# Optimization experiments

Measured on AMD Instinct MI355X. Metric: run time of the kernel, lower is better.

Reference implementation:

```python
import jax, jax.numpy as jnp
import numpy as np

N_QUBITS = 8


def setup_inputs() -> dict:
    key = jax.random.key(0)
    k1, k2, k3, k4 = jax.random.split(key, 4)
    B, S, E, F = 4, 4096, 1024, 4096
    x = jax.random.normal(k1, (B, S, E), dtype=jnp.float32)
    theta = jax.random.normal(k2, (N_QUBITS,), dtype=jnp.float32)
    # nn.Linear default init scale ~ 1/sqrt(fan_in)
    w1 = jax.random.normal(k3, (F, N_QUBITS), dtype=jnp.float32) / np.sqrt(N_QUBITS)
    w2 = jax.random.normal(k4, (E, F), dtype=jnp.float32) / np.sqrt(F)
    return {"x": x, "theta": theta, "w1": w1, "w2": w2}


def reference(x, theta, w1, w2):
    # Quantum circuit per wire i: |0> -RX(x_i)-> -RY(theta_i)-> <Z>
    # No entangling gates, so <Z_i> = cos(x_i) * cos(theta_i) exactly.
    q_vecs = jnp.cos(x[..., :N_QUBITS]) * jnp.cos(theta)  # [B,S,nq]
    h = jax.nn.relu(jnp.einsum('bsq,fq->bsf', q_vecs, w1))  # [B,S,F]
    # dropout is identity in eval mode
    out = jnp.einsum('bsf,ef->bse', h, w2)  # [B,S,E]
    return out
```

## Files before the change

### kernel.cpp

```cpp
#include <hip/hip_runtime.h>
#include <hip/hip_bf16.h>


#define M_TOTAL 16384
#define E_DIM 1024
#define F_DIM 4096
#define NQ 8

typedef __attribute__((ext_vector_type(8))) short bf16x8;
typedef __attribute__((ext_vector_type(8))) unsigned short ushort8;
typedef __attribute__((ext_vector_type(4))) float f32x4;

__device__ __forceinline__ unsigned short f2bf(float f) {
  union { float f; unsigned u; } c; c.f = f;
  unsigned u = c.u + (0x7fffu + ((c.u >> 16) & 1u));
  return (unsigned short)(u >> 16);
}

__global__ __launch_bounds__(256) void w2cvt_kernel(
    const float* __restrict__ w2, unsigned short* __restrict__ w2bf) {
  size_t i = ((size_t)blockIdx.x * 256 + threadIdx.x) * 8;
  float v[8];
  *(float4*)&v[0] = *(const float4*)&w2[i];
  *(float4*)&v[4] = *(const float4*)&w2[i + 4];
  ushort8 p;
#pragma unroll
  for (int j = 0; j < 8; ++j) p[j] = f2bf(v[j]);
  *(ushort8*)&w2bf[i] = p;
}

__global__ __launch_bounds__(256) void qrelu_kernel(
    const float* __restrict__ x, const float* __restrict__ theta,
    const float* __restrict__ w1, unsigned short* __restrict__ A, int m_base) {
  __shared__ float qv[32][NQ];
  const int t = threadIdx.x;
  const int m0 = m_base + blockIdx.x * 32;
  {
    const int ml = t >> 3, q = t & 7;
    float xv = x[(size_t)(m0 + ml) * 1024 + q];
    qv[ml][q] = cosf(xv) * cosf(theta[q]);
  }
  __syncthreads();

  for (int oi = 0; oi < 2; ++oi) {
    const int o = t + oi * 256;
    float w[64];
#pragma unroll
    for (int i = 0; i < 16; ++i)
      *(float4*)&w[i * 4] = *(const float4*)&w1[o * 64 + i * 4];
    for (int ml = 0; ml < 32; ++ml) {
      ushort8 pk;
#pragma unroll
      for (int j = 0; j < 8; ++j) {
        float s = 0.f;
#pragma unroll
        for (int q = 0; q < NQ; ++q) s = fmaf(qv[ml][q], w[j * 8 + q], s);
        pk[j] = f2bf(s > 0.f ? s : 0.f);
      }
      *(ushort8*)&A[(size_t)(m0 - m_base + ml) * F_DIM + o * 8] = pk;
    }
  }
}

#define PHASE(ms, ns, B, W) do { \
  __builtin_amdgcn_s_barrier(); \
  asm volatile("s_waitcnt lgkmcnt(" #W ")" ::: "memory"); \
  __builtin_amdgcn_sched_barrier(0); \
  __builtin_amdgcn_s_setprio(1); \
  _Pragma("unroll") \
  for (int mt2 = 0; mt2 < 4; ++mt2) { \
    _Pragma("unroll") \
    for (int nt2 = 0; nt2 < 2; ++nt2) { \
      _Pragma("unroll") \
      for (int kk = 0; kk < 2; ++kk) { \
        acc[(ms) * 4 + mt2][(ns) * 2 + nt2] = \
            __builtin_amdgcn_mfma_f32_16x16x32_bf16( \
                af[mt2][kk], B[nt2][kk], acc[(ms) * 4 + mt2][(ns) * 2 + nt2], \
                0, 0, 0); \
      } } } \
  __builtin_amdgcn_s_setprio(0); \
  __builtin_amdgcn_s_barrier(); \
} while (0)

#define RD_A(buf, ms) do { \
  _Pragma("unroll") \
  for (int mt2 = 0; mt2 < 4; ++mt2) { \
    af[mt2][0] = *(const bf16x8*)&asW[(buf) * 16384 + (ms) * 4096 + mt2 * 1024 + aO0]; \
    af[mt2][1] = *(const bf16x8*)&asW[(buf) * 16384 + (ms) * 4096 + mt2 * 1024 + aO1]; \
  } } while (0)

#define RD_B(buf, ns, B) do { \
  _Pragma("unroll") \
  for (int nt2 = 0; nt2 < 2; ++nt2) { \
    B[nt2][0] = *(const bf16x8*)&bsW[(buf) * 16384 + (ns) * 2048 + nt2 * 1024 + bO0]; \
    B[nt2][1] = *(const bf16x8*)&bsW[(buf) * 16384 + (ns) * 2048 + nt2 * 1024 + bO1]; \
  } } while (0)

__global__ __launch_bounds__(512, 2) void gemm8_kernel(
    const unsigned short* __restrict__ Abf, const unsigned short* __restrict__ w2bf,
    float* __restrict__ out, int m_base) {
  __shared__ __align__(16) unsigned short As[2][2][128 * 64];
  __shared__ __align__(16) unsigned short Bs[2][2][128 * 64];

  const int tid = threadIdx.x;
  const int lane = tid & 63;
  const int wid = tid >> 6;
  const int wr = wid >> 2;
  const int wc = wid & 3;

  const int nwg = gridDim.x;
  const int bid = blockIdx.x;
  const int qq = nwg >> 3, rr = nwg & 7;
  const int xcd = bid & 7, sub = bid >> 3;
  const int wgid =
      (xcd < rr ? xcd * (qq + 1) : rr * (qq + 1) + (xcd - rr) * qq) + sub;
  const int mb = wgid >> 2;
  const int nb = wgid & 3;

  const unsigned short* Ag = Abf + (size_t)mb * 256 * F_DIM;
  const unsigned short* Bg = w2bf + (size_t)nb * 256 * F_DIM;

  f32x4 acc[8][4] = {};
  bf16x8 af[4][2], blo[2][2], bhi[2][2];

  const int hi4 = lane >> 4, l7 = lane & 7, l15 = lane & 15;
  const int aO0 = l15 * 64 + ((hi4 ^ l7) << 3);
  const int aO1 = aO0 ^ 32;
  const int bO0 = ((wc & 1) * 64 + l15) * 64 + ((hi4 ^ l7) << 3);
  const int bO1 = bO0 ^ 32;
  const unsigned short* asW = &As[0][wr][0];
  const unsigned short* bsW = &Bs[0][wc >> 1][0];

  const int srow = tid >> 3;
  const int sc = (tid & 7) ^ (srow & 7);
  const unsigned short* pA0 = Ag + (size_t)(srow)*F_DIM + sc * 8;
  const unsigned short* pA1 = Ag + (size_t)(64 + srow) * F_DIM + sc * 8;
  const unsigned short* pA2 = Ag + (size_t)(128 + srow) * F_DIM + sc * 8;
  const unsigned short* pA3 = Ag + (size_t)(192 + srow) * F_DIM + sc * 8;
  const unsigned short* pB0 = Bg + (size_t)(srow)*F_DIM + sc * 8;
  const unsigned short* pB1 = Bg + (size_t)(64 + srow) * F_DIM + sc * 8;
  const unsigned short* pB2 = Bg + (size_t)(128 + srow) * F_DIM + sc * 8;
  const unsigned short* pB3 = Bg + (size_t)(192 + srow) * F_DIM + sc * 8;

  auto stA = [&](int buf, int half, const unsigned short*& r0,
                 const unsigned short*& r1) {
    unsigned short* d = &As[buf][half][wid * 512];
    __builtin_amdgcn_global_load_lds(
        (const __attribute__((address_space(1))) void*)r0,
        (__attribute__((address_space(3))) void*)d, 16, 0, 0);
    __builtin_amdgcn_global_load_lds(
        (const __attribute__((address_space(1))) void*)r1,
        (__attribute__((address_space(3))) void*)(d + 4096), 16, 0, 0);
    r0 += 64; r1 += 64;
  };
  auto stB = [&](int buf, int half, const unsigned short*& r0,
                 const unsigned short*& r1) {
    unsigned short* d = &Bs[buf][half][wid * 512];
    __builtin_amdgcn_global_load_lds(
        (const __attribute__((address_space(1))) void*)r0,
        (__attribute__((address_space(3))) void*)d, 16, 0, 0);
    __builtin_amdgcn_global_load_lds(
        (const __attribute__((address_space(1))) void*)r1,
        (__attribute__((address_space(3))) void*)(d + 4096), 16, 0, 0);
    r0 += 64; r1 += 64;
  };

  stB(0, 0, pB0, pB1); stB(0, 1, pB2, pB3);
  stA(0, 0, pA0, pA1); stA(0, 1, pA2, pA3);
  stB(1, 0, pB0, pB1); stB(1, 1, pB2, pB3);
  stA(1, 0, pA0, pA1);
  asm volatile("s_waitcnt vmcnt(6)" ::: "memory");
  __builtin_amdgcn_s_barrier();

#pragma unroll 1
  for (int it = 0; it < F_DIM / 128; ++it) {
    const bool notlast = (it != F_DIM / 128 - 1);
    RD_A(0, 0); RD_B(0, 0, blo); RD_B(0, 1, bhi);
    stA(1, 1, pA2, pA3);
    PHASE(0, 0, blo, 4);
    PHASE(0, 1, bhi, 0);
    RD_A(0, 1);
    if (notlast) stB(0, 0, pB0, pB1);
    PHASE(1, 1, bhi, 0);
    if (notlast) {
      stB(0, 1, pB2, pB3);
      stA(0, 0, pA0, pA1);
      asm volatile("s_waitcnt vmcnt(6)" ::: "memory");
    } else {
      asm volatile("s_waitcnt vmcnt(0)" ::: "memory");
    }
    PHASE(1, 0, blo, 0);
    RD_A(1, 0); RD_B(1, 0, blo); RD_B(1, 1, bhi);
    if (notlast) stA(0, 1, pA2, pA3);
    PHASE(0, 0, blo, 4);
    PHASE(0, 1, bhi, 0);
    RD_A(1, 1);
    if (notlast) stB(1, 0, pB0, pB1);
    PHASE(1, 1, bhi, 0);
    if (notlast) {
      stB(1, 1, pB2, pB3);
      stA(1, 0, pA0, pA1);
      asm volatile("s_waitcnt vmcnt(6)" ::: "memory");
    }
    PHASE(1, 0, blo, 0);
  }

  const int cl = lane & 15, rg = lane >> 4;
  float* ob = out + (size_t)(m_base + mb * 256 + wr * 128) * E_DIM + nb * 256 +
              wc * 64 + cl;
#pragma unroll
  for (int mt = 0; mt < 8; ++mt)
#pragma unroll
    for (int r = 0; r < 4; ++r) {
      float* orow = ob + (size_t)(mt * 16 + rg * 4 + r) * E_DIM;
#pragma unroll
      for (int nt = 0; nt < 4; ++nt) orow[nt * 16] = acc[mt][nt][r];
    }
}

extern "C" void kernel_launch(void* const* d_in, const int* in_sizes, int n_in,
                              void* d_out, int out_size, void* d_ws, size_t ws_size,
                              hipStream_t stream) {
  const float* x = (const float*)d_in[0];
  const float* theta = (const float*)d_in[1];
  const float* w1 = (const float*)d_in[2];
  const float* w2 = (const float*)d_in[3];
  float* out = (float*)d_out;

  unsigned short* w2bf = (unsigned short*)d_ws;
  unsigned short* A = w2bf + (size_t)E_DIM * F_DIM;

  size_t abytes = ws_size - (size_t)E_DIM * F_DIM * 2;
  size_t maxrows = abytes / ((size_t)F_DIM * 2);
  int Mc = (int)((maxrows / 256) * 256);
  if (Mc > M_TOTAL) Mc = M_TOTAL;
  if (Mc < 256) Mc = 256;

  w2cvt_kernel<<<E_DIM * F_DIM / 2048, 256, 0, stream>>>(w2, w2bf);

  for (int mb = 0; mb < M_TOTAL; mb += Mc) {
    int rows = M_TOTAL - mb < Mc ? M_TOTAL - mb : Mc;
    qrelu_kernel<<<rows / 32, 256, 0, stream>>>(x, theta, w1, A, mb);
    gemm8_kernel<<<(rows / 256) * 4, 512, 0, stream>>>(A, w2bf, out, mb);
  }
}
```

Measured before the change: 167.3 us.

## Switch GEMM to 32x32x16 MFMA with reworked LDS pipeline schedule

Replaces the 16x16x32 bf16 MFMA tiling with 32x32x16 MFMA tiles, so each wave holds 4x2 accumulators of 16 floats. The LDS fragment read pattern, swizzle offsets and epilogue store mapping change to match. The double-buffered schedule is restructured into K-substeps with ping-pong register fragments and a full vmcnt/lgkmcnt sync before restaging each buffer. The aim is fewer MFMA issues and fewer LDS reads per FLOP. In exchange it adds full-drain sync points that may expose global load latency.

Result: no change. 167.4 us (+0.1%).

```diff
diff --git a/kernel.cpp b/kernel.cpp
--- a/kernel.cpp
+++ b/kernel.cpp
@@ -9,7 +9,7 @@
 
 typedef __attribute__((ext_vector_type(8))) short bf16x8;
 typedef __attribute__((ext_vector_type(8))) unsigned short ushort8;
-typedef __attribute__((ext_vector_type(4))) float f32x4;
+typedef __attribute__((ext_vector_type(16))) float f32x16;
 
 __device__ __forceinline__ unsigned short f2bf(float f) {
   union { float f; unsigned u; } c; c.f = f;
@@ -62,45 +62,62 @@
   }
 }
 
-#define PHASE(ms, ns, B, W) do { \
-  __builtin_amdgcn_s_barrier(); \
-  asm volatile("s_waitcnt lgkmcnt(" #W ")" ::: "memory"); \
-  __builtin_amdgcn_sched_barrier(0); \
+#define READ_STEP(b, aO, bO, pp) do { \
+  fA[pp][0] = *(const bf16x8*)&As[(b)*16384 + 0*2048 + (aO)]; \
+  fA[pp][1] = *(const bf16x8*)&As[(b)*16384 + 1*2048 + (aO)]; \
+  fA[pp][2] = *(const bf16x8*)&As[(b)*16384 + 2*2048 + (aO)]; \
+  fA[pp][3] = *(const bf16x8*)&As[(b)*16384 + 3*2048 + (aO)]; \
+  fB[pp][0] = *(const bf16x8*)&Bs[(b)*16384 + 0*2048 + (bO)]; \
+  fB[pp][1] = *(const bf16x8*)&Bs[(b)*16384 + 1*2048 + (bO)]; \
+} while (0)
+
+#define MFMA_STEP(pp) do { \
   __builtin_amdgcn_s_setprio(1); \
   _Pragma("unroll") \
-  for (int mt2 = 0; mt2 < 4; ++mt2) { \
+  for (int mt = 0; mt < 4; ++mt) \
     _Pragma("unroll") \
-    for (int nt2 = 0; nt2 < 2; ++nt2) { \
-      _Pragma("unroll") \
-      for (int kk = 0; kk < 2; ++kk) { \
-        acc[(ms) * 4 + mt2][(ns) * 2 + nt2] = \
-            __builtin_amdgcn_mfma_f32_16x16x32_bf16( \
-                af[mt2][kk], B[nt2][kk], acc[(ms) * 4 + mt2][(ns) * 2 + nt2], \
-                0, 0, 0); \
-      } } } \
+    for (int nt = 0; nt < 2; ++nt) \
+      acc[mt][nt] = __builtin_amdgcn_mfma_f32_32x32x16_bf16( \
+          fA[pp][mt], fB[pp][nt], acc[mt][nt], 0, 0, 0); \
   __builtin_amdgcn_s_setprio(0); \
+} while (0)
+
+#define W6 do { \
+  asm volatile("s_waitcnt lgkmcnt(6)" ::: "memory"); \
+  __builtin_amdgcn_sched_barrier(0); \
+} while (0)
+
+#define SYNC_POINT do { \
+  asm volatile("s_waitcnt vmcnt(0) lgkmcnt(0)" ::: "memory"); \
   __builtin_amdgcn_s_barrier(); \
 } while (0)
 
-#define RD_A(buf, ms) do { \
-  _Pragma("unroll") \
-  for (int mt2 = 0; mt2 < 4; ++mt2) { \
-    af[mt2][0] = *(const bf16x8*)&asW[(buf) * 16384 + (ms) * 4096 + mt2 * 1024 + aO0]; \
-    af[mt2][1] = *(const bf16x8*)&asW[(buf) * 16384 + (ms) * 4096 + mt2 * 1024 + aO1]; \
-  } } while (0)
-
-#define RD_B(buf, ns, B) do { \
-  _Pragma("unroll") \
-  for (int nt2 = 0; nt2 < 2; ++nt2) { \
-    B[nt2][0] = *(const bf16x8*)&bsW[(buf) * 16384 + (ns) * 2048 + nt2 * 1024 + bO0]; \
-    B[nt2][1] = *(const bf16x8*)&bsW[(buf) * 16384 + (ns) * 2048 + nt2 * 1024 + bO1]; \
-  } } while (0)
-
-__global__ __launch_bounds__(512, 2) void gemm8_kernel(
+#define STAGE(b) do { \
+  __builtin_amdgcn_global_load_lds((const __attribute__((address_space(1))) void*)pA0, \
+      (__attribute__((address_space(3))) void*)&As[(b)*16384 + 0*4096 + wid*512], 16, 0, 0); \
+  __builtin_amdgcn_global_load_lds((const __attribute__((address_space(1))) void*)pA1, \
+      (__attribute__((address_space(3))) void*)&As[(b)*16384 + 1*4096 + wid*512], 16, 0, 0); \
+  __builtin_amdgcn_global_load_lds((const __attribute__((address_space(1))) void*)pA2, \
+      (__attribute__((address_space(3))) void*)&As[(b)*16384 + 2*4096 + wid*512], 16, 0, 0); \
+  __builtin_amdgcn_global_load_lds((const __attribute__((address_space(1))) void*)pA3, \
+      (__attribute__((address_space(3))) void*)&As[(b)*16384 + 3*4096 + wid*512], 16, 0, 0); \
+  __builtin_amdgcn_global_load_lds((const __attribute__((address_space(1))) void*)pB0, \
+      (__attribute__((address_space(3))) void*)&Bs[(b)*16384 + 0*4096 + wid*512], 16, 0, 0); \
+  __builtin_amdgcn_global_load_lds((const __attribute__((address_space(1))) void*)pB1, \
+      (__attribute__((address_space(3))) void*)&Bs[(b)*16384 + 1*4096 + wid*512], 16, 0, 0); \
+  __builtin_amdgcn_global_load_lds((const __attribute__((address_space(1))) void*)pB2, \
+      (__attribute__((address_space(3))) void*)&Bs[(b)*16384 + 2*4096 + wid*512], 16, 0, 0); \
+  __builtin_amdgcn_global_load_lds((const __attribute__((address_space(1))) void*)pB3, \
+      (__attribute__((address_space(3))) void*)&Bs[(b)*16384 + 3*4096 + wid*512], 16, 0, 0); \
+  pA0 += 64; pA1 += 64; pA2 += 64; pA3 += 64; \
+  pB0 += 64; pB1 += 64; pB2 += 64; pB3 += 64; \
+} while (0)
+
+__global__ __launch_bounds__(512, 2) void gemm32_kernel(
     const unsigned short* __restrict__ Abf, const unsigned short* __restrict__ w2bf,
     float* __restrict__ out, int m_base) {
-  __shared__ __align__(16) unsigned short As[2][2][128 * 64];
-  __shared__ __align__(16) unsigned short Bs[2][2][128 * 64];
+  __shared__ __align__(16) unsigned short As[2 * 16384];
+  __shared__ __align__(16) unsigned short Bs[2 * 16384];
 
   const int tid = threadIdx.x;
   const int lane = tid & 63;
@@ -120,16 +137,20 @@
   const unsigned short* Ag = Abf + (size_t)mb * 256 * F_DIM;
   const unsigned short* Bg = w2bf + (size_t)nb * 256 * F_DIM;
 
-  f32x4 acc[8][4] = {};
-  bf16x8 af[4][2], blo[2][2], bhi[2][2];
-
-  const int hi4 = lane >> 4, l7 = lane & 7, l15 = lane & 15;
-  const int aO0 = l15 * 64 + ((hi4 ^ l7) << 3);
-  const int aO1 = aO0 ^ 32;
-  const int bO0 = ((wc & 1) * 64 + l15) * 64 + ((hi4 ^ l7) << 3);
-  const int bO1 = bO0 ^ 32;
-  const unsigned short* asW = &As[0][wr][0];
-  const unsigned short* bsW = &Bs[0][wc >> 1][0];
+  f32x16 acc[4][2] = {};
+  bf16x8 fA[2][4], fB[2][2];
+
+  const int hi = lane >> 5, l31 = lane & 31, l7 = lane & 7;
+  const int aBase = wr * 8192 + l31 * 64;
+  const int aO0 = aBase + (((hi + 0) ^ l7) << 3);
+  const int aO1 = aBase + (((hi + 2) ^ l7) << 3);
+  const int aO2 = aBase + (((hi + 4) ^ l7) << 3);
+  const int aO3 = aBase + (((hi + 6) ^ l7) << 3);
+  const int bBase = (wc >> 1) * 8192 + ((wc & 1) * 64 + l31) * 64;
+  const int bO0 = bBase + (((hi + 0) ^ l7) << 3);
+  const int bO1 = bBase + (((hi + 2) ^ l7) << 3);
+  const int bO2 = bBase + (((hi + 4) ^ l7) << 3);
+  const int bO3 = bBase + (((hi + 6) ^ l7) << 3);
 
   const int srow = tid >> 3;
   const int sc = (tid & 7) ^ (srow & 7);
@@ -142,80 +163,50 @@
   const unsigned short* pB2 = Bg + (size_t)(128 + srow) * F_DIM + sc * 8;
   const unsigned short* pB3 = Bg + (size_t)(192 + srow) * F_DIM + sc * 8;
 
-  auto stA = [&](int buf, int half, const unsigned short*& r0,
-                 const unsigned short*& r1) {
-    unsigned short* d = &As[buf][half][wid * 512];
-    __builtin_amdgcn_global_load_lds(
-        (const __attribute__((address_space(1))) void*)r0,
-        (__attribute__((address_space(3))) void*)d, 16, 0, 0);
-    __builtin_amdgcn_global_load_lds(
-        (const __attribute__((address_space(1))) void*)r1,
-        (__attribute__((address_space(3))) void*)(d + 4096), 16, 0, 0);
-    r0 += 64; r1 += 64;
-  };
-  auto stB = [&](int buf, int half, const unsigned short*& r0,
-                 const unsigned short*& r1) {
-    unsigned short* d = &Bs[buf][half][wid * 512];
-    __builtin_amdgcn_global_load_lds(
-        (const __attribute__((address_space(1))) void*)r0,
-        (__attribute__((address_space(3))) void*)d, 16, 0, 0);
-    __builtin_amdgcn_global_load_lds(
-        (const __attribute__((address_space(1))) void*)r1,
-        (__attribute__((address_space(3))) void*)(d + 4096), 16, 0, 0);
-    r0 += 64; r1 += 64;
-  };
-
-  stB(0, 0, pB0, pB1); stB(0, 1, pB2, pB3);
-  stA(0, 0, pA0, pA1); stA(0, 1, pA2, pA3);
-  stB(1, 0, pB0, pB1); stB(1, 1, pB2, pB3);
-  stA(1, 0, pA0, pA1);
-  asm volatile("s_waitcnt vmcnt(6)" ::: "memory");
+  STAGE(0);
+  STAGE(1);
+  asm volatile("s_waitcnt vmcnt(8)" ::: "memory");
   __builtin_amdgcn_s_barrier();
+  READ_STEP(0, aO0, bO0, 0);
 
 #pragma unroll 1
-  for (int it = 0; it < F_DIM / 128; ++it) {
-    const bool notlast = (it != F_DIM / 128 - 1);
-    RD_A(0, 0); RD_B(0, 0, blo); RD_B(0, 1, bhi);
-    stA(1, 1, pA2, pA3);
-    PHASE(0, 0, blo, 4);
-    PHASE(0, 1, bhi, 0);
-    RD_A(0, 1);
-    if (notlast) stB(0, 0, pB0, pB1);
-    PHASE(1, 1, bhi, 0);
-    if (notlast) {
-      stB(0, 1, pB2, pB3);
-      stA(0, 0, pA0, pA1);
-      asm volatile("s_waitcnt vmcnt(6)" ::: "memory");
-    } else {
-      asm volatile("s_waitcnt vmcnt(0)" ::: "memory");
+  for (int it = 0; it < 32; ++it) {
+    const bool nl = (it < 31);
+    READ_STEP(0, aO1, bO1, 1);
+    W6; MFMA_STEP(0);
+    READ_STEP(0, aO2, bO2, 0);
+    W6; MFMA_STEP(1);
+    READ_STEP(0, aO3, bO3, 1);
+    W6; MFMA_STEP(0);
+    SYNC_POINT;
+    if (nl) STAGE(0);
+    READ_STEP(1, aO0, bO0, 0);
+    W6; MFMA_STEP(1);
+    READ_STEP(1, aO1, bO1, 1);
+    W6; MFMA_STEP(0);
+    READ_STEP(1, aO2, bO2, 0);
+    W6; MFMA_STEP(1);
+    READ_STEP(1, aO3, bO3, 1);
+    W6; MFMA_STEP(0);
+    SYNC_POINT;
+    if (nl) {
+      STAGE(1);
+      READ_STEP(0, aO0, bO0, 0);
     }
-    PHASE(1, 0, blo, 0);
-    RD_A(1, 0); RD_B(1, 0, blo); RD_B(1, 1, bhi);
-    if (notlast) stA(0, 1, pA2, pA3);
-    PHASE(0, 0, blo, 4);
-    PHASE(0, 1, bhi, 0);
-    RD_A(1, 1);
-    if (notlast) stB(1, 0, pB0, pB1);
-    PHASE(1, 1, bhi, 0);
-    if (notlast) {
-      stB(1, 1, pB2, pB3);
-      stA(1, 0, pA0, pA1);
-      asm volatile("s_waitcnt vmcnt(6)" ::: "memory");
-    }
-    PHASE(1, 0, blo, 0);
-  }
-
-  const int cl = lane & 15, rg = lane >> 4;
+    W6; MFMA_STEP(1);
+  }
+
   float* ob = out + (size_t)(m_base + mb * 256 + wr * 128) * E_DIM + nb * 256 +
-              wc * 64 + cl;
-#pragma unroll
-  for (int mt = 0; mt < 8; ++mt)
-#pragma unroll
-    for (int r = 0; r < 4; ++r) {
-      float* orow = ob + (size_t)(mt * 16 + rg * 4 + r) * E_DIM;
-#pragma unroll
-      for (int nt = 0; nt < 4; ++nt) orow[nt * 16] = acc[mt][nt][r];
-    }
+              wc * 64 + l31;
+#pragma unroll
+  for (int mt = 0; mt < 4; ++mt)
+#pragma unroll
+    for (int nt = 0; nt < 2; ++nt)
+#pragma unroll
+      for (int r = 0; r < 16; ++r) {
+        const int row = mt * 32 + (r & 3) + 8 * (r >> 2) + 4 * hi;
+        ob[(size_t)row * E_DIM + nt * 32] = acc[mt][nt][r];
+      }
 }
 
 extern "C" void kernel_launch(void* const* d_in, const int* in_sizes, int n_in,
@@ -241,6 +232,6 @@
   for (int mb = 0; mb < M_TOTAL; mb += Mc) {
     int rows = M_TOTAL - mb < Mc ? M_TOTAL - mb : Mc;
     qrelu_kernel<<<rows / 32, 256, 0, stream>>>(x, theta, w1, A, mb);
-    gemm8_kernel<<<(rows / 256) * 4, 512, 0, stream>>>(A, w2bf, out, mb);
-  }
-}
+    gemm32_kernel<<<(rows / 256) * 4, 512, 0, stream>>>(A, w2bf, out, mb);
+  }
+}
```

## Double-buffer LDS fragment registers and cut barriers in GEMM main loop

Applied to the files above, without the earlier changes.

The main GEMM loop now alternates between two register sets for the A and B-low fragments, so the LDS reads for the next phase are issued before the current phase's MFMAs. It drops the trailing barrier from each phase and reorders the global-to-LDS staging, with adjusted vmcnt/lgkmcnt wait counts. The aim is to hide LDS read latency behind MFMA work and lower synchronisation overhead. In exchange it uses more VGPRs, which may threaten the two-blocks-per-CU occupancy, and relies on hand-tuned wait counts whose correctness is fragile.

Result: slower. 221.8 us (+32.6%).

```diff
diff --git a/kernel.cpp b/kernel.cpp
--- a/kernel.cpp
+++ b/kernel.cpp
@@ -62,8 +62,12 @@
   }
 }
 
-#define PHASE(ms, ns, B, W) do { \
-  __builtin_amdgcn_s_barrier(); \
+#define BAR __builtin_amdgcn_s_barrier()
+#define SB __builtin_amdgcn_sched_barrier(0)
+#define VM(n) asm volatile("s_waitcnt vmcnt(" #n ")" ::: "memory")
+
+#define PHASE(AF, BF, ms, ns, W) do { \
+  BAR; \
   asm volatile("s_waitcnt lgkmcnt(" #W ")" ::: "memory"); \
   __builtin_amdgcn_sched_barrier(0); \
   __builtin_amdgcn_s_setprio(1); \
@@ -75,25 +79,25 @@
       for (int kk = 0; kk < 2; ++kk) { \
         acc[(ms) * 4 + mt2][(ns) * 2 + nt2] = \
             __builtin_amdgcn_mfma_f32_16x16x32_bf16( \
-                af[mt2][kk], B[nt2][kk], acc[(ms) * 4 + mt2][(ns) * 2 + nt2], \
+                AF[mt2][kk], BF[nt2][kk], acc[(ms) * 4 + mt2][(ns) * 2 + nt2], \
                 0, 0, 0); \
       } } } \
   __builtin_amdgcn_s_setprio(0); \
-  __builtin_amdgcn_s_barrier(); \
+  __builtin_amdgcn_sched_barrier(0); \
 } while (0)
 
-#define RD_A(buf, ms) do { \
+#define RD_A(buf, ms, AF) do { \
   _Pragma("unroll") \
   for (int mt2 = 0; mt2 < 4; ++mt2) { \
-    af[mt2][0] = *(const bf16x8*)&asW[(buf) * 16384 + (ms) * 4096 + mt2 * 1024 + aO0]; \
-    af[mt2][1] = *(const bf16x8*)&asW[(buf) * 16384 + (ms) * 4096 + mt2 * 1024 + aO1]; \
+    AF[mt2][0] = *(const bf16x8*)&asW[(buf) * 16384 + (ms) * 4096 + mt2 * 1024 + aO0]; \
+    AF[mt2][1] = *(const bf16x8*)&asW[(buf) * 16384 + (ms) * 4096 + mt2 * 1024 + aO1]; \
   } } while (0)
 
-#define RD_B(buf, ns, B) do { \
+#define RD_B(buf, ns, BF) do { \
   _Pragma("unroll") \
   for (int nt2 = 0; nt2 < 2; ++nt2) { \
-    B[nt2][0] = *(const bf16x8*)&bsW[(buf) * 16384 + (ns) * 2048 + nt2 * 1024 + bO0]; \
-    B[nt2][1] = *(const bf16x8*)&bsW[(buf) * 16384 + (ns) * 2048 + nt2 * 1024 + bO1]; \
+    BF[nt2][0] = *(const bf16x8*)&bsW[(buf) * 16384 + (ns) * 2048 + nt2 * 1024 + bO0]; \
+    BF[nt2][1] = *(const bf16x8*)&bsW[(buf) * 16384 + (ns) * 2048 + nt2 * 1024 + bO1]; \
   } } while (0)
 
 __global__ __launch_bounds__(512, 2) void gemm8_kernel(
@@ -121,7 +125,7 @@
   const unsigned short* Bg = w2bf + (size_t)nb * 256 * F_DIM;
 
   f32x4 acc[8][4] = {};
-  bf16x8 af[4][2], blo[2][2], bhi[2][2];
+  bf16x8 afP[4][2], afQ[4][2], bloP[2][2], bloQ[2][2], bhi[2][2];
 
   const int hi4 = lane >> 4, l7 = lane & 7, l15 = lane & 15;
   const int aO0 = l15 * 64 + ((hi4 ^ l7) << 3);
@@ -167,42 +171,43 @@
 
   stB(0, 0, pB0, pB1); stB(0, 1, pB2, pB3);
   stA(0, 0, pA0, pA1); stA(0, 1, pA2, pA3);
-  stB(1, 0, pB0, pB1); stB(1, 1, pB2, pB3);
-  stA(1, 0, pA0, pA1);
-  asm volatile("s_waitcnt vmcnt(6)" ::: "memory");
-  __builtin_amdgcn_s_barrier();
+  stA(1, 0, pA0, pA1); stA(1, 1, pA2, pA3);
+  VM(4);
+  BAR;
+  RD_A(0, 0, afP); RD_B(0, 0, bloP);
 
 #pragma unroll 1
-  for (int it = 0; it < F_DIM / 128; ++it) {
-    const bool notlast = (it != F_DIM / 128 - 1);
-    RD_A(0, 0); RD_B(0, 0, blo); RD_B(0, 1, bhi);
-    stA(1, 1, pA2, pA3);
-    PHASE(0, 0, blo, 4);
-    PHASE(0, 1, bhi, 0);
-    RD_A(0, 1);
-    if (notlast) stB(0, 0, pB0, pB1);
-    PHASE(1, 1, bhi, 0);
-    if (notlast) {
-      stB(0, 1, pB2, pB3);
-      stA(0, 0, pA0, pA1);
-      asm volatile("s_waitcnt vmcnt(6)" ::: "memory");
-    } else {
-      asm volatile("s_waitcnt vmcnt(0)" ::: "memory");
+  for (int it = 0; it < 32; ++it) {
+    const bool s2 = (it < 31);
+    RD_B(0, 1, bhi);
+    stB(1, 0, pB0, pB1);
+    PHASE(afP, bloP, 0, 0, 4);  BAR;
+    RD_A(0, 1, afQ);
+    stB(1, 1, pB2, pB3);
+    PHASE(afP, bhi, 0, 1, 8);   BAR;
+    if (s2) stA(0, 0, pA0, pA1);
+    PHASE(afQ, bhi, 1, 1, 0);
+    if (s2) { VM(2); } else { VM(0); }
+    BAR;
+    RD_A(1, 0, afP); RD_B(1, 0, bloQ);
+    if (s2) stA(0, 1, pA2, pA3);
+    PHASE(afQ, bloP, 1, 0, 12); BAR;
+
+    RD_B(1, 1, bhi);
+    if (s2) stB(0, 0, pB0, pB1);
+    PHASE(afP, bloQ, 0, 0, 4);  BAR;
+    RD_A(1, 1, afQ);
+    if (s2) stB(0, 1, pB2, pB3);
+    PHASE(afP, bhi, 0, 1, 8);   BAR;
+    if (s2) stA(1, 0, pA0, pA1);
+    PHASE(afQ, bhi, 1, 1, 0);
+    if (s2) VM(2);
+    BAR;
+    if (s2) {
+      RD_A(0, 0, afP); RD_B(0, 0, bloP);
+      stA(1, 1, pA2, pA3);
     }
-    PHASE(1, 0, blo, 0);
-    RD_A(1, 0); RD_B(1, 0, blo); RD_B(1, 1, bhi);
-    if (notlast) stA(0, 1, pA2, pA3);
-    PHASE(0, 0, blo, 4);
-    PHASE(0, 1, bhi, 0);
-    RD_A(1, 1);
-    if (notlast) stB(1, 0, pB0, pB1);
-    PHASE(1, 1, bhi, 0);
-    if (notlast) {
-      stB(1, 1, pB2, pB3);
-      stA(1, 0, pA0, pA1);
-      asm volatile("s_waitcnt vmcnt(6)" ::: "memory");
-    }
-    PHASE(1, 0, blo, 0);
+    PHASE(afQ, bloQ, 1, 0, 12); BAR;
   }
 
   const int cl = lane & 15, rg = lane >> 4;
```
